# Kernel tuning notes

Measured on AMD Instinct MI355X. Metric: run time of the kernel, lower is better.

The kernel has to match this reference:

```python
import jax, jax.numpy as jnp
import numpy as np

D = 16      # input_dim (state dimension)
H = 64      # hidden width
B = 32768   # batch size


def setup_inputs() -> dict:
    key = jax.random.key(0)
    ks = jax.random.split(key, 16)
    inp = {
        "ts": jnp.arange(3, dtype=jnp.float32),          # output times [0, 1, 2]
        "x0": jax.random.normal(ks[0], (B, D), jnp.float32),
    }
    dims = [(D, H), (H, H), (H, H), (H, D)]
    i = 1
    for l, (din, dout) in enumerate(dims):
        inp[f"W{l}"] = jax.random.normal(ks[i], (din, dout), jnp.float32) / np.sqrt(din).astype(np.float32)
        inp[f"b{l}"] = jnp.zeros((dout,), jnp.float32)
        inp[f"g{l}"] = jax.random.normal(ks[i + 1], (dout,), jnp.float32) * 0.1   # hyper_gate weight (Linear(1,dout))
        inp[f"gb{l}"] = jnp.zeros((dout,), jnp.float32)                            # hyper_gate bias
        inp[f"hb{l}"] = jax.random.normal(ks[i + 2], (dout,), jnp.float32) * 0.1   # hyper_bias weight (no bias)
        i += 3
    return inp


def reference(ts, x0,
              W0, b0, g0, gb0, hb0,
              W1, b1, g1, gb1, hb1,
              W2, b2, g2, gb2, hb2,
              W3, b3, g3, gb3, hb3):
    layers = [(W0, b0, g0, gb0, hb0), (W1, b1, g1, gb1, hb1),
              (W2, b2, g2, gb2, hb2), (W3, b3, g3, gb3, hb3)]
    n_layers = len(layers)

    def odenet(t, x):
        # ConcatSquashLinear: (x@W + b) * sigmoid(t*g + gb) + t*hb, tanh between layers
        h = x
        for l, (W, b, g, gb, hb) in enumerate(layers):
            h = (h @ W + b) * jax.nn.sigmoid(t * g + gb) + t * hb
            if l < n_layers - 1:
                h = jnp.tanh(h)
        return h

    def odefunc(t, z):
        # z: [B, D+2]; last two channels accumulate log-det and kinetic energy
        x = z[:, :D]
        f = lambda xx: odenet(t, xx)
        dx = f(x)
        # exact divergence = trace of Jacobian, via D forward-mode JVPs
        eye = jnp.eye(D, dtype=x.dtype)
        Jv = jax.vmap(lambda e: jax.jvp(f, (x,), (jnp.broadcast_to(e, x.shape),))[1])(eye)  # [D, B, D]
        dl = jnp.einsum('ibi->b', Jv)                  # trace per sample
        dv = 0.5 * jnp.sum(dx * dx, axis=1)            # kinetic energy density
        return jnp.concatenate([dx, dl[:, None], dv[:, None]], axis=1)

    z0 = jnp.pad(x0, ((0, 0), (0, 2)))  # F.pad(x0, (0,2)) with zeros

    def rk4_step(z, t_pair):
        t0, t1 = t_pair
        h = t1 - t0
        k1 = odefunc(t0, z)
        k2 = odefunc(t0 + 0.5 * h, z + 0.5 * h * k1)
        k3 = odefunc(t0 + 0.5 * h, z + 0.5 * h * k2)
        k4 = odefunc(t1, z + h * k3)
        zn = z + (h / 6.0) * (k1 + 2.0 * k2 + 2.0 * k3 + k4)
        return zn, zn

    _, zs_tail = jax.lax.scan(rk4_step, z0, (ts[:-1], ts[1:]))
    zs = jnp.concatenate([z0[None], zs_tail], axis=0)   # [T, B, D+2]

    xs = zs[:, :, :-2]
    log_det = zs[-1, :, -2]
    loss_L = jnp.abs(zs[-1, :, -1])
    return xs, log_det, loss_L, jnp.zeros_like(loss_L)
```

## Files before the change

kernel.cpp:

```cpp
#include <hip/hip_runtime.h>

#define NB 32768
#define DD 16
#define HH 64
#define EPB 16

typedef __attribute__((ext_vector_type(8))) short short8;
typedef __attribute__((ext_vector_type(4))) float f32x4;
typedef __attribute__((ext_vector_type(4))) unsigned uint4v;

union Frag { short8 s; uint4v u; unsigned d[4]; };

struct Params {
  const float *ts, *x0;
  const float *W0,*b0,*g0,*gb0,*hb0;
  const float *W1,*b1,*g1,*gb1,*hb1;
  const float *W2,*b2,*g2,*gb2,*hb2;
  const float *W3,*b3,*g3,*gb3,*hb3;
  float *out;
};

__device__ __forceinline__ float bfs(unsigned short u){
  return __uint_as_float(((unsigned)u)<<16);
}
__device__ __forceinline__ unsigned short f2bf(float f){
  unsigned u=__float_as_uint(f);
  return (unsigned short)((u + 0x7FFFu + ((u>>16)&1u))>>16);
}
__device__ __forceinline__ unsigned pk2bf(float lo, float hi){
  unsigned a=__float_as_uint(lo)+0x8000u;
  unsigned b=__float_as_uint(hi)+0x8000u;
  return __builtin_amdgcn_perm(b, a, 0x07060302u);
}
__device__ __forceinline__ unsigned short f2bf1(float f){
  return (unsigned short)((__float_as_uint(f)+0x8000u)>>16);
}
__device__ __forceinline__ float sigm(float u){
  return __builtin_amdgcn_rcpf(1.0f+__builtin_amdgcn_exp2f(-1.44269504f*u));
}
#define WV() __builtin_amdgcn_wave_barrier()
#define MFMA(A,B,C) __builtin_amdgcn_mfma_f32_16x16x32_bf16((A),(B),(C),0,0,0)

__device__ __forceinline__ void fwd_epi(const f32x4& c, float tcur,
    float gc, float gbc, float hbc,
    unsigned short* __restrict__ hdst, unsigned short* __restrict__ sdst,
    int jw, int q)
{
  const float gate = sigm(tcur*gc+gbc);
  const float gk   = gate*2.88539008f;
  const float tbk  = (tcur*hbc)*2.88539008f;
  const float g4   = 4.0f*gate;
  #pragma unroll
  for(int r=0;r<4;++r){
    const int el=q*4+r;
    const float preK = c[r]*gk + tbk;
    const float e    = __builtin_amdgcn_exp2f(preK);
    const float rc   = __builtin_amdgcn_rcpf(1.0f+e);
    const float th   = __builtin_fmaf(-2.0f,rc,1.0f);
    hdst[el*72+jw] = f2bf1(th);
    const float sv   = (g4*rc)*(1.0f-rc);
    sdst[el*72+jw] = f2bf1(sv);
  }
}

__global__ __launch_bounds__(256,2) void traj_kernel(Params p){
  __shared__ __align__(16) unsigned short w0b[DD][72];
  __shared__ __align__(16) unsigned short w3t[DD][72];
  __shared__ __align__(16) float xbuf[DD][20];
  __shared__ __align__(16) unsigned short hbh[2][EPB][72];
  __shared__ __align__(16) unsigned short sb[3][EPB][72];
  __shared__ float dxw[4][EPB][17];
  __shared__ __align__(16) float sig3w[4][DD];
  __shared__ __align__(16) unsigned short vt[4][DD][72];

  const int tid = threadIdx.x;
  const int e   = tid>>4;
  const int a   = tid&15;
  const int wv  = tid>>6;
  const int lane= tid&63;
  const int m   = lane&15;
  const int q   = lane>>4;
  const int b   = blockIdx.x*EPB + e;
  const int jw  = wv*16 + m;

  short8 f0fr, f1fr[2], f2fr[2], b3fr[2];
  short8 b1fr[2][4], b2fr[2][4];
  {
    #pragma unroll
    for(int j=0;j<8;++j){
      const int k=q*8+j;
      f0fr[j]=(k<DD)?(short)f2bf(p.W0[k*HH+jw]):(short)0;
    }
    #pragma unroll
    for(int kk=0;kk<2;++kk){
      #pragma unroll
      for(int j=0;j<8;++j){
        const int k=kk*32+q*8+j;
        f1fr[kk][j]=(short)f2bf(p.W1[k*HH+jw]);
        f2fr[kk][j]=(short)f2bf(p.W2[k*HH+jw]);
        b3fr[kk][j]=(short)f2bf(p.W3[k*DD+m]);
      }
      #pragma unroll
      for(int nt=0;nt<4;++nt){
        #pragma unroll
        for(int j=0;j<8;++j){
          const int k=kk*32+q*8+j;
          b1fr[kk][nt][j]=(short)f2bf(p.W1[k*HH+4*m+nt]);
          b2fr[kk][nt][j]=(short)f2bf(p.W2[k*HH+4*m+nt]);
        }
      }
    }
  }
  const float bc0=p.b0[jw], gc0=p.g0[jw], gbc0=p.gb0[jw], hbc0=p.hb0[jw];
  const float bc1=p.b1[jw], gc1=p.g1[jw], gbc1=p.gb1[jw], hbc1=p.hb1[jw];
  const float bc2=p.b2[jw], gc2=p.g2[jw], gbc2=p.gb2[jw], hbc2=p.hb2[jw];
  const float bc3=p.b3[m],  gc3=p.g3[m],  gbc3=p.gb3[m],  hbc3=p.hb3[m];

  for(int idx=tid; idx<DD*HH; idx+=256) w0b[idx>>6][idx&63]=f2bf(p.W0[idx]);
  for(int idx=tid; idx<HH*DD; idx+=256) w3t[idx&15][idx>>4]=f2bf(p.W3[idx]);
  __syncthreads();

  float zbx = p.x0[b*DD+a];
  p.out[b*DD+a]=zbx;
  float trp[4]={0.f,0.f,0.f,0.f};
  float dvp=0.f;

  #pragma unroll 1
  for(int step=0; step<2; ++step){
    const float t0=p.ts[step], t1=p.ts[step+1];
    const float hs=t1-t0;
    float dzx=0.f;
    float zwx=zbx;
    #pragma unroll 1
    for(int stage=0; stage<4; ++stage){
      const float cin=(stage==0)?0.f:((stage==3)?1.f:0.5f);
      const float tcur=t0+cin*hs;
      const float wg=(stage==0||stage==3)?1.f:2.f;
      const float fs=hs*(1.f/6.f)*wg;
      const float fs5=0.5f*fs;

      xbuf[e][a]=zwx;
      __syncthreads();

      f32x4 c={bc0,bc0,bc0,bc0};
      {
        Frag xh, xl; xh.s=short8{0,0,0,0,0,0,0,0}; xl.s=xh.s;
        if(q<2){
          const float4 xa=*reinterpret_cast<const float4*>(&xbuf[m][q*8]);
          const float4 xb=*reinterpret_cast<const float4*>(&xbuf[m][q*8+4]);
          const float xv[8]={xa.x,xa.y,xa.z,xa.w,xb.x,xb.y,xb.z,xb.w};
          #pragma unroll
          for(int d=0;d<4;++d){
            const unsigned u0=__float_as_uint(xv[2*d]), u1=__float_as_uint(xv[2*d+1]);
            xh.d[d]=__builtin_amdgcn_perm(u1,u0,0x07060302u);
            const float l0=xv[2*d]-__uint_as_float(u0&0xFFFF0000u);
            const float l1=xv[2*d+1]-__uint_as_float(u1&0xFFFF0000u);
            xl.d[d]=pk2bf(l0,l1);
          }
        }
        c=MFMA(xh.s,f0fr,c); c=MFMA(xl.s,f0fr,c);
      }
      fwd_epi(c,tcur,gc0,gbc0,hbc0,&hbh[0][0][0],&sb[0][0][0],jw,q);
      __syncthreads();

      c=f32x4{bc1,bc1,bc1,bc1};
      #pragma unroll
      for(int kk=0;kk<2;++kk){
        const short8 ah=*reinterpret_cast<const short8*>(&hbh[0][m][kk*32+q*8]);
        c=MFMA(ah,f1fr[kk],c);
      }
      fwd_epi(c,tcur,gc1,gbc1,hbc1,&hbh[1][0][0],&sb[1][0][0],jw,q);
      __syncthreads();

      c=f32x4{bc2,bc2,bc2,bc2};
      #pragma unroll
      for(int kk=0;kk<2;++kk){
        const short8 ah=*reinterpret_cast<const short8*>(&hbh[1][m][kk*32+q*8]);
        c=MFMA(ah,f2fr[kk],c);
      }
      fwd_epi(c,tcur,gc2,gbc2,hbc2,&hbh[0][0][0],&sb[2][0][0],jw,q);
      __syncthreads();

      c=f32x4{bc3,bc3,bc3,bc3};
      #pragma unroll
      for(int kk=0;kk<2;++kk){
        const short8 ah=*reinterpret_cast<const short8*>(&hbh[0][m][kk*32+q*8]);
        c=MFMA(ah,b3fr[kk],c);
      }
      const float gate3=sigm(tcur*gc3+gbc3);
      {
        const float tb=tcur*hbc3;
        #pragma unroll
        for(int r=0;r<4;++r)
          dxw[wv][q*4+r][m]=c[r]*gate3+tb;
        if(q==0) sig3w[wv][m]=gate3;
      }
      WV();
      const float dxk=dxw[wv][e][a];
      dvp += fs5*dxk*dxk;

      float tf[4][4];
      {
        const float4 sg4=*reinterpret_cast<const float4*>(&sig3w[wv][q*4]);
        #pragma unroll
        for(int r=0;r<4;++r){
          const ushort4 w4=*reinterpret_cast<const ushort4*>(&w3t[q*4+r][4*m]);
          const float sg=(&sg4.x)[r];
          tf[r][0]=sg*bfs(w4.x); tf[r][1]=sg*bfs(w4.y);
          tf[r][2]=sg*bfs(w4.z); tf[r][3]=sg*bfs(w4.w);
        }
      }

      #pragma unroll
      for(int el=0; el<4; ++el){
        const int ee=wv*4+el;
        Frag a0[2];
        #pragma unroll
        for(int kk=0;kk<2;++kk){
          const uint4v wd=*reinterpret_cast<const uint4v*>(&w0b[m][kk*32+q*8]);
          const uint4v sd=*reinterpret_cast<const uint4v*>(&sb[0][ee][kk*32+q*8]);
          #pragma unroll
          for(int d=0;d<4;++d){
            const unsigned w2d=wd[d], s2d=sd[d];
            const float wlo=__uint_as_float(w2d<<16), whi=__uint_as_float(w2d&0xFFFF0000u);
            const float slo=__uint_as_float(s2d<<16), shi=__uint_as_float(s2d&0xFFFF0000u);
            a0[kk].d[d]=pk2bf(wlo*slo,whi*shi);
          }
        }
        f32x4 c1[4]={{0,0,0,0},{0,0,0,0},{0,0,0,0},{0,0,0,0}};
        #pragma unroll
        for(int kk=0;kk<2;++kk){
          #pragma unroll
          for(int nt=0;nt<4;++nt)
            c1[nt]=MFMA(a0[kk].s,b1fr[kk][nt],c1[nt]);
        }
        {
          const ushort4 s1v=*reinterpret_cast<const ushort4*>(&sb[1][ee][4*m]);
          const float sc0=bfs(s1v.x),sc1=bfs(s1v.y),sc2=bfs(s1v.z),sc3=bfs(s1v.w);
          #pragma unroll
          for(int r=0;r<4;++r){
            uint2 dw;
            dw.x=pk2bf(c1[0][r]*sc0, c1[1][r]*sc1);
            dw.y=pk2bf(c1[2][r]*sc2, c1[3][r]*sc3);
            *reinterpret_cast<uint2*>(&vt[wv][q*4+r][4*m])=dw;
          }
        }
        WV();
        short8 a2[2];
        #pragma unroll
        for(int kk=0;kk<2;++kk)
          a2[kk]=*reinterpret_cast<const short8*>(&vt[wv][m][kk*32+q*8]);
        f32x4 c2[4]={{0,0,0,0},{0,0,0,0},{0,0,0,0},{0,0,0,0}};
        #pragma unroll
        for(int kk=0;kk<2;++kk){
          #pragma unroll
          for(int nt=0;nt<4;++nt)
            c2[nt]=MFMA(a2[kk],b2fr[kk][nt],c2[nt]);
        }
        {
          const ushort4 s2v=*reinterpret_cast<const ushort4*>(&sb[2][ee][4*m]);
          const float s20=bfs(s2v.x),s21=bfs(s2v.y),s22=bfs(s2v.z),s23=bfs(s2v.w);
          float d0=c2[0][0]*tf[0][0]+c2[0][1]*tf[1][0]+c2[0][2]*tf[2][0]+c2[0][3]*tf[3][0];
          float d1=c2[1][0]*tf[0][1]+c2[1][1]*tf[1][1]+c2[1][2]*tf[2][1]+c2[1][3]*tf[3][1];
          float d2=c2[2][0]*tf[0][2]+c2[2][1]*tf[1][2]+c2[2][2]*tf[2][2]+c2[2][3]*tf[3][2];
          float d3=c2[3][0]*tf[0][3]+c2[3][1]*tf[1][3]+c2[3][2]*tf[2][3]+c2[3][3]*tf[3][3];
          const float tr=d0*s20+d1*s21+d2*s22+d3*s23;
          trp[el] += fs*tr;
        }
        WV();
      }

      dzx += fs*dxk;
      const float cn=(stage==2)?1.f:0.5f;
      if(stage<3) zwx=zbx+cn*hs*dxk;
    }
    zbx += dzx;
    p.out[(step+1)*(NB*DD)+b*DD+a]=zbx;
  }

  #pragma unroll
  for(int el=0; el<4; ++el){
    float v=trp[el];
    #pragma unroll
    for(int mk=32;mk>=1;mk>>=1) v+=__shfl_xor(v,mk,64);
    if(lane==el) p.out[3*NB*DD + blockIdx.x*EPB + wv*4 + el]=v;
  }
  {
    float v=dvp;
    #pragma unroll
    for(int mk=8;mk>=1;mk>>=1) v+=__shfl_xor(v,mk,16);
    if(a==0){
      p.out[3*NB*DD+NB+b]=fabsf(v);
      p.out[3*NB*DD+2*NB+b]=0.f;
    }
  }
}

extern "C" void kernel_launch(void* const* d_in, const int* in_sizes, int n_in,
                              void* d_out, int out_size, void* d_ws, size_t ws_size,
                              hipStream_t stream){
  Params p;
  p.ts  = (const float*)d_in[0];
  p.x0  = (const float*)d_in[1];
  p.W0  = (const float*)d_in[2];  p.b0 =(const float*)d_in[3];
  p.g0  = (const float*)d_in[4];  p.gb0=(const float*)d_in[5];  p.hb0=(const float*)d_in[6];
  p.W1  = (const float*)d_in[7];  p.b1 =(const float*)d_in[8];
  p.g1  = (const float*)d_in[9];  p.gb1=(const float*)d_in[10]; p.hb1=(const float*)d_in[11];
  p.W2  = (const float*)d_in[12]; p.b2 =(const float*)d_in[13];
  p.g2  = (const float*)d_in[14]; p.gb2=(const float*)d_in[15]; p.hb2=(const float*)d_in[16];
  p.W3  = (const float*)d_in[17]; p.b3 =(const float*)d_in[18];
  p.g3  = (const float*)d_in[19]; p.gb3=(const float*)d_in[20]; p.hb3=(const float*)d_in[21];
  p.out = (float*)d_out;
  hipLaunchKernelGGL(traj_kernel, dim3(NB/EPB), dim3(256), 0, stream, p);
}
```

Before: 253.4 us.

## Store slopes in fp32, pre-split x into bf16 hi/lo, use packed-float math

Tanh-derivative slopes are now kept in fp32 shared memory instead of bf16. Each thread splits the state into bf16 hi and lo halves before the barrier, so the layer-0 MFMA operands are plain LDS loads. W3 is kept transposed in fp32, and the epilogues and trace reduction use 2-wide float vectors to allow packed FMA. Launch bounds rise to 4 blocks per SM to raise occupancy. In exchange, fp32 slope buffers use more LDS, and the tighter register budget may cause spills.

```diff
diff --git a/kernel.cpp b/kernel.cpp
--- a/kernel.cpp
+++ b/kernel.cpp
@@ -6,6 +6,7 @@
 #define EPB 16
 
 typedef __attribute__((ext_vector_type(8))) short short8;
+typedef __attribute__((ext_vector_type(2))) float f32x2;
 typedef __attribute__((ext_vector_type(4))) float f32x4;
 typedef __attribute__((ext_vector_type(4))) unsigned uint4v;
 
@@ -20,9 +21,6 @@
   float *out;
 };
 
-__device__ __forceinline__ float bfs(unsigned short u){
-  return __uint_as_float(((unsigned)u)<<16);
-}
 __device__ __forceinline__ unsigned short f2bf(float f){
   unsigned u=__float_as_uint(f);
   return (unsigned short)((u + 0x7FFFu + ((u>>16)&1u))>>16);
@@ -32,6 +30,11 @@
   unsigned b=__float_as_uint(hi)+0x8000u;
   return __builtin_amdgcn_perm(b, a, 0x07060302u);
 }
+__device__ __forceinline__ unsigned pk2bf2(f32x2 v){
+  unsigned a=__float_as_uint(v[0])+0x8000u;
+  unsigned b=__float_as_uint(v[1])+0x8000u;
+  return __builtin_amdgcn_perm(b, a, 0x07060302u);
+}
 __device__ __forceinline__ unsigned short f2bf1(float f){
   return (unsigned short)((__float_as_uint(f)+0x8000u)>>16);
 }
@@ -43,34 +46,45 @@
 
 __device__ __forceinline__ void fwd_epi(const f32x4& c, float tcur,
     float gc, float gbc, float hbc,
-    unsigned short* __restrict__ hdst, unsigned short* __restrict__ sdst,
+    unsigned short* __restrict__ hdst, float* __restrict__ sdst,
     int jw, int q)
 {
   const float gate = sigm(tcur*gc+gbc);
   const float gk   = gate*2.88539008f;
   const float tbk  = (tcur*hbc)*2.88539008f;
   const float g4   = 4.0f*gate;
-  #pragma unroll
-  for(int r=0;r<4;++r){
-    const int el=q*4+r;
-    const float preK = c[r]*gk + tbk;
-    const float e    = __builtin_amdgcn_exp2f(preK);
-    const float rc   = __builtin_amdgcn_rcpf(1.0f+e);
-    const float th   = __builtin_fmaf(-2.0f,rc,1.0f);
-    hdst[el*72+jw] = f2bf1(th);
-    const float sv   = (g4*rc)*(1.0f-rc);
-    sdst[el*72+jw] = f2bf1(sv);
-  }
-}
-
-__global__ __launch_bounds__(256,2) void traj_kernel(Params p){
+  const f32x2 c01={c[0],c[1]}, c23={c[2],c[3]};
+  const f32x2 pre01 = c01*gk + tbk;
+  const f32x2 pre23 = c23*gk + tbk;
+  const f32x2 e01={__builtin_amdgcn_exp2f(pre01[0]),__builtin_amdgcn_exp2f(pre01[1])};
+  const f32x2 e23={__builtin_amdgcn_exp2f(pre23[0]),__builtin_amdgcn_exp2f(pre23[1])};
+  const f32x2 d01=e01+1.0f, d23=e23+1.0f;
+  const f32x2 rc01={__builtin_amdgcn_rcpf(d01[0]),__builtin_amdgcn_rcpf(d01[1])};
+  const f32x2 rc23={__builtin_amdgcn_rcpf(d23[0]),__builtin_amdgcn_rcpf(d23[1])};
+  const f32x2 th01 = rc01*-2.0f + 1.0f;
+  const f32x2 th23 = rc23*-2.0f + 1.0f;
+  const f32x2 om01 = 1.0f - rc01, om23 = 1.0f - rc23;
+  const f32x2 sv01 = (rc01*g4)*om01, sv23 = (rc23*g4)*om23;
+  const int el0=q*4;
+  hdst[(el0+0)*72+jw]=f2bf1(th01[0]);
+  hdst[(el0+1)*72+jw]=f2bf1(th01[1]);
+  hdst[(el0+2)*72+jw]=f2bf1(th23[0]);
+  hdst[(el0+3)*72+jw]=f2bf1(th23[1]);
+  sdst[(el0+0)*68+jw]=sv01[0];
+  sdst[(el0+1)*68+jw]=sv01[1];
+  sdst[(el0+2)*68+jw]=sv23[0];
+  sdst[(el0+3)*68+jw]=sv23[1];
+}
+
+__global__ __launch_bounds__(256,4) void traj_kernel(Params p){
   __shared__ __align__(16) unsigned short w0b[DD][72];
-  __shared__ __align__(16) unsigned short w3t[DD][72];
-  __shared__ __align__(16) float xbuf[DD][20];
+  __shared__ __align__(16) float w3tt[HH][20];
+  __shared__ __align__(16) unsigned short xh[DD][40];
+  __shared__ __align__(16) unsigned short xl[DD][40];
   __shared__ __align__(16) unsigned short hbh[2][EPB][72];
-  __shared__ __align__(16) unsigned short sb[3][EPB][72];
-  __shared__ float dxw[4][EPB][17];
+  __shared__ __align__(16) float sbf[3][EPB][68];
   __shared__ __align__(16) float sig3w[4][DD];
+  __shared__ __align__(16) float dxs[4][4][17];
   __shared__ __align__(16) unsigned short vt[4][DD][72];
 
   const int tid = threadIdx.x;
@@ -117,7 +131,12 @@
   const float bc3=p.b3[m],  gc3=p.g3[m],  gbc3=p.gb3[m],  hbc3=p.hb3[m];
 
   for(int idx=tid; idx<DD*HH; idx+=256) w0b[idx>>6][idx&63]=f2bf(p.W0[idx]);
-  for(int idx=tid; idx<HH*DD; idx+=256) w3t[idx&15][idx>>4]=f2bf(p.W3[idx]);
+  for(int idx=tid; idx<HH*DD; idx+=256) w3tt[idx>>4][idx&15]=p.W3[idx];
+  if(tid<128){
+    const int mm=tid>>3, dd=8+(tid&7);
+    reinterpret_cast<unsigned*>(xh)[mm*20+dd]=0;
+    reinterpret_cast<unsigned*>(xl)[mm*20+dd]=0;
+  }
   __syncthreads();
 
   float zbx = p.x0[b*DD+a];
@@ -139,28 +158,20 @@
       const float fs=hs*(1.f/6.f)*wg;
       const float fs5=0.5f*fs;
 
-      xbuf[e][a]=zwx;
+      {
+        const unsigned ux=__float_as_uint(zwx);
+        xh[e][a]=(unsigned short)(ux>>16);
+        xl[e][a]=f2bf1(zwx-__uint_as_float(ux&0xFFFF0000u));
+      }
       __syncthreads();
 
       f32x4 c={bc0,bc0,bc0,bc0};
       {
-        Frag xh, xl; xh.s=short8{0,0,0,0,0,0,0,0}; xl.s=xh.s;
-        if(q<2){
-          const float4 xa=*reinterpret_cast<const float4*>(&xbuf[m][q*8]);
-          const float4 xb=*reinterpret_cast<const float4*>(&xbuf[m][q*8+4]);
-          const float xv[8]={xa.x,xa.y,xa.z,xa.w,xb.x,xb.y,xb.z,xb.w};
-          #pragma unroll
-          for(int d=0;d<4;++d){
-            const unsigned u0=__float_as_uint(xv[2*d]), u1=__float_as_uint(xv[2*d+1]);
-            xh.d[d]=__builtin_amdgcn_perm(u1,u0,0x07060302u);
-            const float l0=xv[2*d]-__uint_as_float(u0&0xFFFF0000u);
-            const float l1=xv[2*d+1]-__uint_as_float(u1&0xFFFF0000u);
-            xl.d[d]=pk2bf(l0,l1);
-          }
-        }
-        c=MFMA(xh.s,f0fr,c); c=MFMA(xl.s,f0fr,c);
-      }
-      fwd_epi(c,tcur,gc0,gbc0,hbc0,&hbh[0][0][0],&sb[0][0][0],jw,q);
+        const short8 ah=*reinterpret_cast<const short8*>(&xh[m][q*8]);
+        const short8 al=*reinterpret_cast<const short8*>(&xl[m][q*8]);
+        c=MFMA(ah,f0fr,c); c=MFMA(al,f0fr,c);
+      }
+      fwd_epi(c,tcur,gc0,gbc0,hbc0,&hbh[0][0][0],&sbf[0][0][0],jw,q);
       __syncthreads();
 
       c=f32x4{bc1,bc1,bc1,bc1};
@@ -169,7 +180,7 @@
         const short8 ah=*reinterpret_cast<const short8*>(&hbh[0][m][kk*32+q*8]);
         c=MFMA(ah,f1fr[kk],c);
       }
-      fwd_epi(c,tcur,gc1,gbc1,hbc1,&hbh[1][0][0],&sb[1][0][0],jw,q);
+      fwd_epi(c,tcur,gc1,gbc1,hbc1,&hbh[1][0][0],&sbf[1][0][0],jw,q);
       __syncthreads();
 
       c=f32x4{bc2,bc2,bc2,bc2};
@@ -178,7 +189,7 @@
         const short8 ah=*reinterpret_cast<const short8*>(&hbh[1][m][kk*32+q*8]);
         c=MFMA(ah,f2fr[kk],c);
       }
-      fwd_epi(c,tcur,gc2,gbc2,hbc2,&hbh[0][0][0],&sb[2][0][0],jw,q);
+      fwd_epi(c,tcur,gc2,gbc2,hbc2,&hbh[0][0][0],&sbf[2][0][0],jw,q);
       __syncthreads();
 
       c=f32x4{bc3,bc3,bc3,bc3};
@@ -188,26 +199,26 @@
         c=MFMA(ah,b3fr[kk],c);
       }
       const float gate3=sigm(tcur*gc3+gbc3);
+      const float tb3=tcur*hbc3;
+      if(q==wv){
+        #pragma unroll
+        for(int r=0;r<4;++r)
+          dxs[wv][r][m]=c[r]*gate3+tb3;
+      }
+      if(q==0) sig3w[wv][m]=gate3;
+      WV();
+      const float dxk=dxs[wv][q][m];
+      dvp += fs5*dxk*dxk;
+
+      f32x2 tf2[4][2];
       {
-        const float tb=tcur*hbc3;
-        #pragma unroll
-        for(int r=0;r<4;++r)
-          dxw[wv][q*4+r][m]=c[r]*gate3+tb;
-        if(q==0) sig3w[wv][m]=gate3;
-      }
-      WV();
-      const float dxk=dxw[wv][e][a];
-      dvp += fs5*dxk*dxk;
-
-      float tf[4][4];
-      {
-        const float4 sg4=*reinterpret_cast<const float4*>(&sig3w[wv][q*4]);
-        #pragma unroll
-        for(int r=0;r<4;++r){
-          const ushort4 w4=*reinterpret_cast<const ushort4*>(&w3t[q*4+r][4*m]);
-          const float sg=(&sg4.x)[r];
-          tf[r][0]=sg*bfs(w4.x); tf[r][1]=sg*bfs(w4.y);
-          tf[r][2]=sg*bfs(w4.z); tf[r][3]=sg*bfs(w4.w);
+        const f32x4 sg4=*reinterpret_cast<const f32x4*>(&sig3w[wv][q*4]);
+        const f32x2 sgA={sg4[0],sg4[1]}, sgB={sg4[2],sg4[3]};
+        #pragma unroll
+        for(int nt=0;nt<4;++nt){
+          const f32x4 w4=*reinterpret_cast<const f32x4*>(&w3tt[4*m+nt][q*4]);
+          tf2[nt][0]=sgA*f32x2{w4[0],w4[1]};
+          tf2[nt][1]=sgB*f32x2{w4[2],w4[3]};
         }
       }
 
@@ -218,13 +229,14 @@
         #pragma unroll
         for(int kk=0;kk<2;++kk){
           const uint4v wd=*reinterpret_cast<const uint4v*>(&w0b[m][kk*32+q*8]);
-          const uint4v sd=*reinterpret_cast<const uint4v*>(&sb[0][ee][kk*32+q*8]);
+          const f32x4 sA=*reinterpret_cast<const f32x4*>(&sbf[0][ee][kk*32+q*8]);
+          const f32x4 sB=*reinterpret_cast<const f32x4*>(&sbf[0][ee][kk*32+q*8+4]);
           #pragma unroll
           for(int d=0;d<4;++d){
-            const unsigned w2d=wd[d], s2d=sd[d];
-            const float wlo=__uint_as_float(w2d<<16), whi=__uint_as_float(w2d&0xFFFF0000u);
-            const float slo=__uint_as_float(s2d<<16), shi=__uint_as_float(s2d&0xFFFF0000u);
-            a0[kk].d[d]=pk2bf(wlo*slo,whi*shi);
+            const unsigned w2d=wd[d];
+            const f32x2 w2={__uint_as_float(w2d<<16),__uint_as_float(w2d&0xFFFF0000u)};
+            const f32x2 s2=(d<2)? f32x2{sA[2*d],sA[2*d+1]} : f32x2{sB[2*d-4],sB[2*d-3]};
+            a0[kk].d[d]=pk2bf2(w2*s2);
           }
         }
         f32x4 c1[4]={{0,0,0,0},{0,0,0,0},{0,0,0,0},{0,0,0,0}};
@@ -235,13 +247,14 @@
             c1[nt]=MFMA(a0[kk].s,b1fr[kk][nt],c1[nt]);
         }
         {
-          const ushort4 s1v=*reinterpret_cast<const ushort4*>(&sb[1][ee][4*m]);
-          const float sc0=bfs(s1v.x),sc1=bfs(s1v.y),sc2=bfs(s1v.z),sc3=bfs(s1v.w);
+          const f32x4 s1v=*reinterpret_cast<const f32x4*>(&sbf[1][ee][4*m]);
+          const f32x4 pr0=c1[0]*s1v[0], pr1=c1[1]*s1v[1];
+          const f32x4 pr2=c1[2]*s1v[2], pr3=c1[3]*s1v[3];
           #pragma unroll
           for(int r=0;r<4;++r){
             uint2 dw;
-            dw.x=pk2bf(c1[0][r]*sc0, c1[1][r]*sc1);
-            dw.y=pk2bf(c1[2][r]*sc2, c1[3][r]*sc3);
+            dw.x=pk2bf(pr0[r],pr1[r]);
+            dw.y=pk2bf(pr2[r],pr3[r]);
             *reinterpret_cast<uint2*>(&vt[wv][q*4+r][4*m])=dw;
           }
         }
@@ -258,13 +271,14 @@
             c2[nt]=MFMA(a2[kk],b2fr[kk][nt],c2[nt]);
         }
         {
-          const ushort4 s2v=*reinterpret_cast<const ushort4*>(&sb[2][ee][4*m]);
-          const float s20=bfs(s2v.x),s21=bfs(s2v.y),s22=bfs(s2v.z),s23=bfs(s2v.w);
-          float d0=c2[0][0]*tf[0][0]+c2[0][1]*tf[1][0]+c2[0][2]*tf[2][0]+c2[0][3]*tf[3][0];
-          float d1=c2[1][0]*tf[0][1]+c2[1][1]*tf[1][1]+c2[1][2]*tf[2][1]+c2[1][3]*tf[3][1];
-          float d2=c2[2][0]*tf[0][2]+c2[2][1]*tf[1][2]+c2[2][2]*tf[2][2]+c2[2][3]*tf[3][2];
-          float d3=c2[3][0]*tf[0][3]+c2[3][1]*tf[1][3]+c2[3][2]*tf[2][3]+c2[3][3]*tf[3][3];
-          const float tr=d0*s20+d1*s21+d2*s22+d3*s23;
+          const f32x4 s2v=*reinterpret_cast<const f32x4*>(&sbf[2][ee][4*m]);
+          float tr=0.f;
+          #pragma unroll
+          for(int nt=0;nt<4;++nt){
+            const f32x2 t = f32x2{c2[nt][0],c2[nt][1]}*tf2[nt][0]
+                          + f32x2{c2[nt][2],c2[nt][3]}*tf2[nt][1];
+            tr += (t[0]+t[1])*s2v[nt];
+          }
           trp[el] += fs*tr;
         }
         WV();
```

Measured after the change: 646.3 us. +155.1%, slower.
